# Performance work log

Hardware: AMD Instinct MI355X
Metric: run time of the kernel (lower is better)

## Reference

```python
import jax, jax.numpy as jnp
import numpy as np

B, N, FDIM = 2, 512, 1024
HEADS, DH = 4, 256          # out_per_head = 1024 // 4
AH = 256                    # attn_hidden
HID, OUT, NCLS = 512, 128, 10
RATIO, TEMP = 0.8, 0.5


def setup_inputs() -> dict:
    key = jax.random.key(0)
    ks = jax.random.split(key, 16)
    g = lambda i, shape, s: (jax.random.normal(ks[i], shape, dtype=jnp.float32) * s)
    return {
        "x": g(0, (B, N, FDIM), 1.0),
        # GATLayer
        "Wg": g(1, (FDIM, FDIM), 0.02),          # linear weight [out,in], no bias
        "attn": g(2, (HEADS, 2 * DH), 0.05),
        # CausalAttNetV1 edge_mlp: Linear(2F,AH) -> ReLU -> Linear(AH,1)
        "W1": g(3, (AH, 2 * FDIM), 0.02),
        "b1": jnp.zeros((AH,), jnp.float32),
        "w2": g(4, (AH,), 0.05),
        "b2": jnp.zeros((), jnp.float32),
        # GCN
        "gc1_w": g(5, (HID, FDIM), 0.03), "gc1_b": jnp.zeros((HID,), jnp.float32),
        "bn1_g": jnp.ones((HID,), jnp.float32), "bn1_b": jnp.zeros((HID,), jnp.float32),
        "gc2_w": g(6, (OUT, HID), 0.04), "gc2_b": jnp.zeros((OUT,), jnp.float32),
        "bn2_g": jnp.ones((OUT,), jnp.float32), "bn2_b": jnp.zeros((OUT,), jnp.float32),
        # classifier
        "cls_w": g(7, (NCLS, OUT), 0.1), "cls_b": jnp.zeros((NCLS,), jnp.float32),
    }


def _batchnorm(h, gamma, beta):
    # BatchNorm1d in training mode over the flattened (B*N, F) dim, biased var.
    m = h.mean(axis=(0, 1))
    v = jnp.mean((h - m) ** 2, axis=(0, 1))
    return (h - m) * jax.lax.rsqrt(v + 1e-5) * gamma + beta


def _forward(x, Wg, attn, W1, b1, w2, b2,
             gc1_w, gc1_b, bn1_g, bn1_b, gc2_w, gc2_b, bn2_g, bn2_b,
             cls_w, cls_b):
    # ---- GATLayer (adj=None) ----
    hp = jnp.einsum('bnf,of->bno', x, Wg)                     # [B,N,1024]
    hp = hp.reshape(B, N, HEADS, DH).transpose(0, 2, 1, 3)     # [B,H,N,DH]
    a_i, a_j = attn[:, :DH], attn[:, DH:]
    s_i = jnp.einsum('bhnd,hd->bhn', hp, a_i)                  # source score
    s_j = jnp.einsum('bhnd,hd->bhn', hp, a_j)                  # target score
    e = s_i[:, :, :, None] + s_j[:, :, None, :]                # [B,H,N,N]
    e = jnp.where(e >= 0, e, 0.2 * e)                          # LeakyReLU(0.2)
    alpha = jax.nn.softmax(e, axis=-1)
    hn = jnp.einsum('bhij,bhjd->bhid', alpha, hp)
    node_feats = hn.transpose(0, 2, 1, 3).reshape(B, N, HEADS * DH)  # [B,N,1024]

    # ---- CausalAttNetV1 (split cat-linear into row/col halves) ----
    W1i, W1j = W1[:, :FDIM], W1[:, FDIM:]
    pi = jnp.einsum('bnf,af->bna', node_feats, W1i)            # [B,N,AH]
    pj = jnp.einsum('bnf,af->bna', node_feats, W1j)
    hid = jax.nn.relu(pi[:, :, None, :] + pj[:, None, :, :] + b1)  # [B,N,N,AH]
    edge_scores = jnp.einsum('bija,a->bij', hid, w2) + b2      # [B,N,N]
    flat = edge_scores.reshape(B, N * N)
    soft_mask = jax.nn.softmax(flat / TEMP, axis=1)
    k = int(RATIO * N * N)
    thr = jnp.sort(soft_mask, axis=1)[:, -k]                   # k-th largest value
    cm = jnp.where(soft_mask >= thr[:, None], soft_mask, 0.0)
    cm = cm / (cm.sum(axis=1, keepdims=True) + 1e-12)
    causal_adj = cm.reshape(B, N, N)

    # ---- GCN (return_embeddings=True) ----
    h = jnp.einsum('bij,bjf->bif', causal_adj, node_feats)
    h = jnp.einsum('bif,of->bio', h, gc1_w) + gc1_b
    h = jax.nn.relu(_batchnorm(h, bn1_g, bn1_b))
    h = jnp.einsum('bij,bjf->bif', causal_adj, h)
    h = jnp.einsum('bif,of->bio', h, gc2_w) + gc2_b
    h = jax.nn.relu(_batchnorm(h, bn2_g, bn2_b))

    # ---- classify (mode='pred') ----
    feat_causal = h.mean(axis=1)                               # [B,128]
    return jnp.einsum('bf,cf->bc', feat_causal, cls_w) + cls_b # [B,NCLS]


def reference(x, Wg, attn, W1, b1, w2, b2,
              gc1_w, gc1_b, bn1_g, bn1_b, gc2_w, gc2_b, bn2_g, bn2_b,
              cls_w, cls_b):
    return _forward(x, Wg, attn, W1, b1, w2, b2,
                    gc1_w, gc1_b, bn1_g, bn1_b, gc2_w, gc2_b, bn2_g, bn2_b,
                    cls_w, cls_b)
```

## Files before the change

kernel.cpp:

```cpp
#include <hip/hip_runtime.h>
#include <hip/hip_bf16.h>


__global__ __launch_bounds__(256) void gemm64_nt(
    const float* __restrict__ A, const float* __restrict__ Bm, float* __restrict__ C,
    int K, int lda, int ldb, int ldc, const float* __restrict__ bias,
    const float* __restrict__ Bm2, float* __restrict__ C2, const float* __restrict__ bias2,
    int ksplit)
{
    if (ksplit){
        int z = blockIdx.z; A += (size_t)z*K; Bm += (size_t)z*K; if (z) bias = nullptr;
    } else if (blockIdx.z){
        Bm = Bm2; C = C2; bias = bias2;
    }
    __shared__ float As[64][64], Bs[64][64];
    int t = threadIdx.x;
    int m0 = blockIdx.y*64, n0 = blockIdx.x*64;
    int w = t>>6, lane = t&63;
    int mi = lane>>3, ni = lane&7;
    int kc = w*16;
    const float* Ar = A + (size_t)(m0+lane)*lda + kc;
    const float* Br = Bm + (size_t)(n0+lane)*ldb + kc;
    float4 pa[4], pb[4];
    #pragma unroll
    for (int j=0;j<4;++j){ pa[j]=*(const float4*)(Ar+j*4); pb[j]=*(const float4*)(Br+j*4); }
    float acc[8][8] = {};
    for (int k0=0; k0<K; k0+=64){
        #pragma unroll
        for (int j=0;j<4;++j){
            As[kc+j*4+0][lane]=pa[j].x; As[kc+j*4+1][lane]=pa[j].y;
            As[kc+j*4+2][lane]=pa[j].z; As[kc+j*4+3][lane]=pa[j].w;
            Bs[kc+j*4+0][lane]=pb[j].x; Bs[kc+j*4+1][lane]=pb[j].y;
            Bs[kc+j*4+2][lane]=pb[j].z; Bs[kc+j*4+3][lane]=pb[j].w;
        }
        if (k0+64 < K){
            #pragma unroll
            for (int j=0;j<4;++j){
                pa[j]=*(const float4*)(Ar+k0+64+j*4);
                pb[j]=*(const float4*)(Br+k0+64+j*4);
            }
        }
        #pragma unroll
        for (int kk=0; kk<16; ++kk){
            float4 a0=*(const float4*)&As[kc+kk][mi*8], a1=*(const float4*)&As[kc+kk][mi*8+4];
            float4 b0=*(const float4*)&Bs[kc+kk][ni*8], b1=*(const float4*)&Bs[kc+kk][ni*8+4];
            float am[8]={a0.x,a0.y,a0.z,a0.w,a1.x,a1.y,a1.z,a1.w};
            float bn[8]={b0.x,b0.y,b0.z,b0.w,b1.x,b1.y,b1.z,b1.w};
            #pragma unroll
            for (int i=0;i<8;++i)
                #pragma unroll
                for (int j2=0;j2<8;++j2) acc[i][j2] += am[i]*bn[j2];
        }
    }
    __syncthreads();
    float* s0 = &As[0][0]; float* s1 = &Bs[0][0];
    if (w>=2){
        float* d = (w==2)? s0 : s1;
        #pragma unroll
        for (int i=0;i<8;++i){
            *(float4*)&d[(mi*8+i)*64+ni*8]   = make_float4(acc[i][0],acc[i][1],acc[i][2],acc[i][3]);
            *(float4*)&d[(mi*8+i)*64+ni*8+4] = make_float4(acc[i][4],acc[i][5],acc[i][6],acc[i][7]);
        }
    }
    __syncthreads();
    if (w<2){
        const float* sv = (w==0)? s0 : s1;
        #pragma unroll
        for (int i=0;i<8;++i){
            float4 v0=*(const float4*)&sv[(mi*8+i)*64+ni*8];
            float4 v1=*(const float4*)&sv[(mi*8+i)*64+ni*8+4];
            acc[i][0]+=v0.x; acc[i][1]+=v0.y; acc[i][2]+=v0.z; acc[i][3]+=v0.w;
            acc[i][4]+=v1.x; acc[i][5]+=v1.y; acc[i][6]+=v1.z; acc[i][7]+=v1.w;
        }
    }
    __syncthreads();
    if (w==1){
        #pragma unroll
        for (int i=0;i<8;++i){
            *(float4*)&s0[(mi*8+i)*64+ni*8]   = make_float4(acc[i][0],acc[i][1],acc[i][2],acc[i][3]);
            *(float4*)&s0[(mi*8+i)*64+ni*8+4] = make_float4(acc[i][4],acc[i][5],acc[i][6],acc[i][7]);
        }
    }
    __syncthreads();
    if (w==0){
        #pragma unroll
        for (int i=0;i<8;++i){
            float4 v0=*(const float4*)&s0[(mi*8+i)*64+ni*8];
            float4 v1=*(const float4*)&s0[(mi*8+i)*64+ni*8+4];
            acc[i][0]+=v0.x; acc[i][1]+=v0.y; acc[i][2]+=v0.z; acc[i][3]+=v0.w;
            acc[i][4]+=v1.x; acc[i][5]+=v1.y; acc[i][6]+=v1.z; acc[i][7]+=v1.w;
        }
        float bb[8];
        #pragma unroll
        for (int j2=0;j2<8;++j2) bb[j2] = bias ? bias[n0+ni*8+j2] : 0.f;
        if (!ksplit){
            #pragma unroll
            for (int i=0;i<8;++i){
                *(float4*)&C[(size_t)(m0+mi*8+i)*ldc + n0+ni*8]   =
                    make_float4(acc[i][0]+bb[0],acc[i][1]+bb[1],acc[i][2]+bb[2],acc[i][3]+bb[3]);
                *(float4*)&C[(size_t)(m0+mi*8+i)*ldc + n0+ni*8+4] =
                    make_float4(acc[i][4]+bb[4],acc[i][5]+bb[5],acc[i][6]+bb[6],acc[i][7]+bb[7]);
            }
        } else {
            #pragma unroll
            for (int i=0;i<8;++i)
                #pragma unroll
                for (int j2=0;j2<8;++j2)
                    atomicAdd(&C[(size_t)(m0+mi*8+i)*ldc + n0+ni*8+j2], acc[i][j2]+bb[j2]);
        }
    }
}

__global__ __launch_bounds__(256) void gemm64_nn(
    const float* __restrict__ A, const float* __restrict__ Bm, float* __restrict__ C,
    int K, int lda, int ldb, int ldc, long sA, long sB, long sC,
    const float* __restrict__ bsc, const float* __restrict__ bsh)
{
    A += (long)blockIdx.z*sA; Bm += (long)blockIdx.z*sB; C += (long)blockIdx.z*sC;
    __shared__ float As[64][64], Bs[64][64];
    int t=threadIdx.x, w=t>>6, lane=t&63;
    int m0=blockIdx.y*64, n0=blockIdx.x*64;
    int mi=lane>>3, ni=lane&7;
    int kc=w*16;
    const float* Ar = A + (size_t)(m0+lane)*lda + kc;
    int kr = lane>>4, nc = (lane&15)*4;
    const float* Br = Bm + (size_t)(kc+kr)*ldb + n0 + nc;
    float4 sc4 = make_float4(1,1,1,1), sh4 = make_float4(0,0,0,0);
    if (bsc){ sc4 = *(const float4*)&bsc[n0+nc]; sh4 = *(const float4*)&bsh[n0+nc]; }
    float4 pa[4], pb[4];
    #pragma unroll
    for (int j=0;j<4;++j){
        pa[j]=*(const float4*)(Ar+j*4);
        pb[j]=*(const float4*)(Br + (size_t)(j*4)*ldb);
    }
    float acc[8][8] = {};
    for (int k0=0; k0<K; k0+=64){
        #pragma unroll
        for (int j=0;j<4;++j){
            As[kc+j*4+0][lane]=pa[j].x; As[kc+j*4+1][lane]=pa[j].y;
            As[kc+j*4+2][lane]=pa[j].z; As[kc+j*4+3][lane]=pa[j].w;
            float4 bv = pb[j];
            if (bsc){
                bv.x=fmaxf(bv.x*sc4.x+sh4.x,0.f); bv.y=fmaxf(bv.y*sc4.y+sh4.y,0.f);
                bv.z=fmaxf(bv.z*sc4.z+sh4.z,0.f); bv.w=fmaxf(bv.w*sc4.w+sh4.w,0.f);
            }
            *(float4*)&Bs[kc+kr+j*4][nc] = bv;
        }
        if (k0+64 < K){
            #pragma unroll
            for (int j=0;j<4;++j){
                pa[j]=*(const float4*)(Ar+k0+64+j*4);
                pb[j]=*(const float4*)(Br + (size_t)(k0+64+j*4)*ldb);
            }
        }
        #pragma unroll
        for (int kk=0; kk<16; ++kk){
            float4 a0=*(const float4*)&As[kc+kk][mi*8], a1=*(const float4*)&As[kc+kk][mi*8+4];
            float4 b0=*(const float4*)&Bs[kc+kk][ni*8], b1=*(const float4*)&Bs[kc+kk][ni*8+4];
            float am[8]={a0.x,a0.y,a0.z,a0.w,a1.x,a1.y,a1.z,a1.w};
            float bn[8]={b0.x,b0.y,b0.z,b0.w,b1.x,b1.y,b1.z,b1.w};
            #pragma unroll
            for (int i=0;i<8;++i)
                #pragma unroll
                for (int j2=0;j2<8;++j2) acc[i][j2] += am[i]*bn[j2];
        }
    }
    __syncthreads();
    float* s0 = &As[0][0]; float* s1 = &Bs[0][0];
    if (w>=2){
        float* d = (w==2)? s0 : s1;
        #pragma unroll
        for (int i=0;i<8;++i){
            *(float4*)&d[(mi*8+i)*64+ni*8]   = make_float4(acc[i][0],acc[i][1],acc[i][2],acc[i][3]);
            *(float4*)&d[(mi*8+i)*64+ni*8+4] = make_float4(acc[i][4],acc[i][5],acc[i][6],acc[i][7]);
        }
    }
    __syncthreads();
    if (w<2){
        const float* sv = (w==0)? s0 : s1;
        #pragma unroll
        for (int i=0;i<8;++i){
            float4 v0=*(const float4*)&sv[(mi*8+i)*64+ni*8];
            float4 v1=*(const float4*)&sv[(mi*8+i)*64+ni*8+4];
            acc[i][0]+=v0.x; acc[i][1]+=v0.y; acc[i][2]+=v0.z; acc[i][3]+=v0.w;
            acc[i][4]+=v1.x; acc[i][5]+=v1.y; acc[i][6]+=v1.z; acc[i][7]+=v1.w;
        }
    }
    __syncthreads();
    if (w==1){
        #pragma unroll
        for (int i=0;i<8;++i){
            *(float4*)&s0[(mi*8+i)*64+ni*8]   = make_float4(acc[i][0],acc[i][1],acc[i][2],acc[i][3]);
            *(float4*)&s0[(mi*8+i)*64+ni*8+4] = make_float4(acc[i][4],acc[i][5],acc[i][6],acc[i][7]);
        }
    }
    __syncthreads();
    if (w==0){
        #pragma unroll
        for (int i=0;i<8;++i){
            float4 v0=*(const float4*)&s0[(mi*8+i)*64+ni*8];
            float4 v1=*(const float4*)&s0[(mi*8+i)*64+ni*8+4];
            acc[i][0]+=v0.x; acc[i][1]+=v0.y; acc[i][2]+=v0.z; acc[i][3]+=v0.w;
            acc[i][4]+=v1.x; acc[i][5]+=v1.y; acc[i][6]+=v1.z; acc[i][7]+=v1.w;
        }
        #pragma unroll
        for (int i=0;i<8;++i){
            *(float4*)&C[(size_t)(m0+mi*8+i)*ldc + n0+ni*8]   =
                make_float4(acc[i][0],acc[i][1],acc[i][2],acc[i][3]);
            *(float4*)&C[(size_t)(m0+mi*8+i)*ldc + n0+ni*8+4] =
                make_float4(acc[i][4],acc[i][5],acc[i][6],acc[i][7]);
        }
    }
}

__global__ void transp_v15(const float* __restrict__ PJ, float* __restrict__ pjT){
    __shared__ float T[64][68];
    int b = blockIdx.z;
    int a0 = blockIdx.x*64, n0 = blockIdx.y*64;
    int t = threadIdx.x;
    int c = t&15, r = t>>4;
    for (int rr=r; rr<64; rr+=16){
        float4 v = *(const float4*)&PJ[(size_t)(b*512+n0+rr)*256 + a0 + c*4];
        T[rr][c*4]=v.x; T[rr][c*4+1]=v.y; T[rr][c*4+2]=v.z; T[rr][c*4+3]=v.w;
    }
    __syncthreads();
    for (int rr=r; rr<64; rr+=16){
        float4 o = make_float4(T[c*4][rr], T[c*4+1][rr], T[c*4+2][rr], T[c*4+3][rr]);
        *(float4*)&pjT[(size_t)b*131072 + (size_t)(a0+rr)*512 + n0 + c*4] = o;
    }
}

__global__ void bnp1(const float* __restrict__ src, float* __restrict__ PS,
                     float* __restrict__ PS2, int F){
    int f0 = blockIdx.x*64, r0 = blockIdx.y*64;
    int fi = threadIdx.x & 63, rg = threadIdx.x >> 6;
    float s=0.f, s2=0.f;
    #pragma unroll
    for (int i=0;i<16;++i){
        float v = src[(size_t)(r0+rg+i*4)*F + f0+fi];
        s += v; s2 += v*v;
    }
    __shared__ float ls[4][64], ls2[4][64];
    ls[rg][fi]=s; ls2[rg][fi]=s2; __syncthreads();
    if (rg==0){
        PS [blockIdx.y*F + f0+fi] = ls[0][fi]+ls[1][fi]+ls[2][fi]+ls[3][fi];
        PS2[blockIdx.y*F + f0+fi] = ls2[0][fi]+ls2[1][fi]+ls2[2][fi]+ls2[3][fi];
    }
}

__global__ void bnp2(const float* __restrict__ PS, const float* __restrict__ PS2,
                     const float* __restrict__ g, const float* __restrict__ be,
                     float* __restrict__ scale, float* __restrict__ shift, int F){
    int f = blockIdx.x*64 + threadIdx.x;
    float S=0.f, S2=0.f;
    #pragma unroll
    for (int c=0;c<16;++c){ S += PS[c*F+f]; S2 += PS2[c*F+f]; }
    float m  = S*(1.f/1024.f);
    float var = S2*(1.f/1024.f) - m*m;
    float sc = g[f] * rsqrtf(var + 1e-5f);
    scale[f]=sc; shift[f]=be[f] - m*sc;
}

__global__ void feat_p(const float* __restrict__ h4, const float* __restrict__ sc,
                       const float* __restrict__ sh, float* __restrict__ featp){
    int b = blockIdx.x, chunk = blockIdx.y;
    int t = threadIdx.x;
    float s = sc[t], o = sh[t], acc = 0.f;
    int n0 = chunk*64;
    #pragma unroll
    for (int i=0;i<64;++i){
        float v = h4[(size_t)(b*512+n0+i)*128 + t]*s + o;
        acc += fmaxf(v, 0.f);
    }
    featp[(b*8+chunk)*128 + t] = acc;
}

__global__ void feat_f(const float* __restrict__ featp, float* __restrict__ feat){
    int b = blockIdx.x, t = threadIdx.x;
    float a = 0.f;
    #pragma unroll
    for (int c=0;c<8;++c) a += featp[(b*8+c)*128 + t];
    feat[b*128+t] = a*(1.f/512.f);
}

__global__ void gemm_nn32(const float* __restrict__ A, const float* __restrict__ Bm,
                          float* __restrict__ C, int K, int lda, int ldb, int ldc,
                          long sA, long sB, long sC,
                          const float* __restrict__ bsc, const float* __restrict__ bsh){
    A  += (long)blockIdx.z * sA;
    Bm += (long)blockIdx.z * sB;
    C  += (long)blockIdx.z * sC;
    __shared__ float As[16][32], Bs[16][64];
    int n0 = blockIdx.x*64, m0 = blockIdx.y*32;
    int t = threadIdx.x, tx = t & 15, ty = t >> 4;
    int sr = t >> 3, sk = (t & 7)*2;
    int bk = t >> 4, bn4 = (t & 15)*4;
    float acc[2][4] = {};
    for (int k0=0; k0<K; k0+=16){
        #pragma unroll
        for (int i=0;i<2;++i) As[sk+i][sr] = A[(size_t)(m0+sr)*lda + k0+sk+i];
        float4 bv = *(const float4*)&Bm[(size_t)(k0+bk)*ldb + n0+bn4];
        if (bsc){
            bv.x = fmaxf(bv.x*bsc[n0+bn4+0]+bsh[n0+bn4+0], 0.f);
            bv.y = fmaxf(bv.y*bsc[n0+bn4+1]+bsh[n0+bn4+1], 0.f);
            bv.z = fmaxf(bv.z*bsc[n0+bn4+2]+bsh[n0+bn4+2], 0.f);
            bv.w = fmaxf(bv.w*bsc[n0+bn4+3]+bsh[n0+bn4+3], 0.f);
        }
        *(float4*)&Bs[bk][bn4] = bv;
        __syncthreads();
        #pragma unroll
        for (int k=0;k<16;++k){
            float a0 = As[k][ty*2], a1 = As[k][ty*2+1];
            float4 b = *(const float4*)&Bs[k][tx*4];
            acc[0][0]+=a0*b.x; acc[0][1]+=a0*b.y; acc[0][2]+=a0*b.z; acc[0][3]+=a0*b.w;
            acc[1][0]+=a1*b.x; acc[1][1]+=a1*b.y; acc[1][2]+=a1*b.z; acc[1][3]+=a1*b.w;
        }
        __syncthreads();
    }
    #pragma unroll
    for (int i=0;i<2;++i){
        float4 v = make_float4(acc[i][0],acc[i][1],acc[i][2],acc[i][3]);
        *(float4*)&C[(size_t)(m0+ty*2+i)*ldc + n0+tx*4] = v;
    }
}

__global__ void gemm_nt32(const float* __restrict__ A, const float* __restrict__ Bm,
                          float* __restrict__ C, int K, int lda, int ldb, int ldc,
                          const float* __restrict__ bias){
    __shared__ float As[16][32], Bs[16][64];
    int n0 = blockIdx.x*64, m0 = blockIdx.y*32;
    int t = threadIdx.x, tx = t & 15, ty = t >> 4;
    int sr = t >> 3, sk = (t & 7)*2;
    int bn = t >> 2, bkk = (t & 3)*4;
    float acc[2][4] = {};
    for (int k0=0; k0<K; k0+=16){
        #pragma unroll
        for (int i=0;i<2;++i) As[sk+i][sr] = A[(size_t)(m0+sr)*lda + k0+sk+i];
        float4 wv = *(const float4*)&Bm[(size_t)(n0+bn)*ldb + k0+bkk];
        Bs[bkk+0][bn]=wv.x; Bs[bkk+1][bn]=wv.y; Bs[bkk+2][bn]=wv.z; Bs[bkk+3][bn]=wv.w;
        __syncthreads();
        #pragma unroll
        for (int k=0;k<16;++k){
            float a0 = As[k][ty*2], a1 = As[k][ty*2+1];
            float4 b = *(const float4*)&Bs[k][tx*4];
            acc[0][0]+=a0*b.x; acc[0][1]+=a0*b.y; acc[0][2]+=a0*b.z; acc[0][3]+=a0*b.w;
            acc[1][0]+=a1*b.x; acc[1][1]+=a1*b.y; acc[1][2]+=a1*b.z; acc[1][3]+=a1*b.w;
        }
        __syncthreads();
    }
    float4 bb = bias ? *(const float4*)&bias[n0+tx*4] : make_float4(0,0,0,0);
    #pragma unroll
    for (int i=0;i<2;++i){
        float4 v = make_float4(acc[i][0]+bb.x,acc[i][1]+bb.y,acc[i][2]+bb.z,acc[i][3]+bb.w);
        *(float4*)&C[(size_t)(m0+ty*2+i)*ldc + n0+tx*4] = v;
    }
}

__global__ void gemm_x_v12(const float* __restrict__ X, const float* __restrict__ Wg,
                           float* __restrict__ dst){
    __shared__ float xs[4][1024];
    int m0 = blockIdx.x*4;
    int t = threadIdx.x;
    for (int i=t;i<4096;i+=256){ int r=i>>10, c=i&1023; xs[r][c]=X[(size_t)(m0+r)*1024+c]; }
    __syncthreads();
    const float* w0 = Wg + (size_t)(t*4)*1024;
    float acc[4][4] = {};
    for (int k0=0;k0<1024;k0+=16){
        float4 xv[4][4];
        #pragma unroll
        for (int r=0;r<4;++r)
            #pragma unroll
            for (int c=0;c<4;++c) xv[r][c] = *(const float4*)&xs[r][k0+4*c];
        #pragma unroll
        for (int j=0;j<4;++j){
            const float* wr = w0 + (size_t)j*1024 + k0;
            #pragma unroll
            for (int c=0;c<4;++c){
                float4 w = *(const float4*)(wr + 4*c);
                #pragma unroll
                for (int r=0;r<4;++r)
                    acc[r][j] += xv[r][c].x*w.x + xv[r][c].y*w.y
                               + xv[r][c].z*w.z + xv[r][c].w*w.w;
            }
        }
    }
    int n0 = t*4;
    #pragma unroll
    for (int r=0;r<4;++r){
        float4 v = make_float4(acc[r][0],acc[r][1],acc[r][2],acc[r][3]);
        *(float4*)&dst[(size_t)(m0+r)*1024 + n0] = v;
    }
}

__global__ void attn_v12(const float* __restrict__ hp, const float* __restrict__ attn,
                         float* __restrict__ nf){
    int blk = blockIdx.x;
    int bh = blk >> 6, i0 = (blk & 63)*8;
    int b = bh >> 2, h = bh & 3;
    int t = threadIdx.x;
    __shared__ float ais[256], ajs[256], sjs[512], sis[8], inv[8];
    __shared__ float alpha[8][512];
    __shared__ float red[256];
    ais[t] = attn[h*512 + t];
    ajs[t] = attn[h*512 + 256 + t];
    __syncthreads();
    const float* hpb = hp + (size_t)b*524288 + h*256;
    for (int j=t; j<512; j+=256){
        const float* row = hpb + (size_t)j*1024;
        float s=0.f;
        for (int d=0; d<256; ++d) s += row[d]*ajs[d];
        sjs[j]=s;
    }
    if (t<8){
        const float* row = hpb + (size_t)(i0+t)*1024;
        float s=0.f;
        for (int d=0; d<256; ++d) s += row[d]*ais[d];
        sis[t]=s;
    }
    __syncthreads();
    for (int ii=0; ii<8; ++ii){
        float si = sis[ii];
        float e0 = si + sjs[t], e1 = si + sjs[t+256];
        e0 = (e0>=0.f)? e0 : 0.2f*e0;
        e1 = (e1>=0.f)? e1 : 0.2f*e1;
        float p0 = expf(e0), p1 = expf(e1);
        alpha[ii][t]=p0; alpha[ii][t+256]=p1;
        red[t]=p0+p1; __syncthreads();
        for (int s=128; s>0; s>>=1){ if (t<s) red[t]+=red[t+s]; __syncthreads(); }
        if (t==0) inv[ii] = 1.0f/red[0];
        __syncthreads();
    }
    float acc[8] = {};
    for (int j=0; j<512; ++j){
        float r = hpb[(size_t)j*1024 + t];
        #pragma unroll
        for (int ii=0; ii<8; ++ii) acc[ii] += alpha[ii][j]*r;
    }
    #pragma unroll
    for (int ii=0; ii<8; ++ii)
        nf[(size_t)(b*512+i0+ii)*1024 + h*256 + t] = acc[ii]*inv[ii];
}

__global__ void sij_v14(const float* __restrict__ hp, const float* __restrict__ attn,
                        float* __restrict__ SI, float* __restrict__ SJ){
    int t = threadIdx.x;
    int lane = t & 63, w = t >> 6;
    int h  = lane >> 4;
    int e0 = (lane & 15) * 16;
    const float* ai = attn + h*512 + e0;
    const float* aj = ai + 256;
    float4 wi[4], wj[4];
    #pragma unroll
    for (int q=0;q<4;++q){ wi[q] = *(const float4*)(ai + 4*q); wj[q] = *(const float4*)(aj + 4*q); }
    int row0 = blockIdx.x*16 + w*4;
    for (int r=0;r<4;++r){
        int row = row0 + r;
        const float* hr = hp + (size_t)row*1024 + h*256 + e0;
        float si=0.f, sj=0.f;
        #pragma unroll
        for (int q=0;q<4;++q){
            float4 v = *(const float4*)(hr + 4*q);
            si += v.x*wi[q].x + v.y*wi[q].y + v.z*wi[q].z + v.w*wi[q].w;
            sj += v.x*wj[q].x + v.y*wj[q].y + v.z*wj[q].z + v.w*wj[q].w;
        }
        #pragma unroll
        for (int s=1;s<16;s<<=1){
            si += __shfl_xor(si, s, 64);
            sj += __shfl_xor(sj, s, 64);
        }
        if ((lane & 15)==0){
            int b = row >> 9, n = row & 511;
            SI[(size_t)(b*4+h)*512 + n] = si;
            SJ[(size_t)(b*4+h)*512 + n] = sj;
        }
    }
}

__global__ __launch_bounds__(512) void attn_pv_v16(const float* __restrict__ hp,
                                                   const float* __restrict__ SI,
                                                   const float* __restrict__ SJ,
                                                   float* __restrict__ nf){
    int blk = blockIdx.x;
    int bh = blk >> 5, i0 = (blk & 31)*16;
    int b = bh >> 2, h = bh & 3;
    int t = threadIdx.x;
    int w = t >> 6, lane = t & 63;
    __shared__ float alpha[16][512];
    __shared__ float wsum[8][16];
    __shared__ float inv[16];
    const float* sjp = SJ + (size_t)bh*512;
    float sj = sjp[t];
    const float* sip = SI + (size_t)bh*512 + i0;
    float part[16];
    #pragma unroll
    for (int ii=0; ii<16; ++ii){
        float e = sip[ii] + sj;
        e = (e>=0.f)? e : 0.2f*e;
        float p = expf(e);
        alpha[ii][t] = p;
        part[ii] = p;
    }
    #pragma unroll
    for (int s=1;s<64;s<<=1){
        #pragma unroll
        for (int ii=0;ii<16;++ii) part[ii] += __shfl_xor(part[ii], s, 64);
    }
    if (lane==0){
        #pragma unroll
        for (int ii=0;ii<16;++ii) wsum[w][ii] = part[ii];
    }
    __syncthreads();
    if (t<16){
        float s=0.f;
        #pragma unroll
        for (int ww=0;ww<8;++ww) s += wsum[ww][t];
        inv[t] = 1.0f/s;
    }
    __syncthreads();
    int d0 = lane*4;
    int iA = w*2;
    const float* hpb = hp + (size_t)b*524288 + h*256 + d0;
    float4 acc0 = make_float4(0,0,0,0), acc1 = make_float4(0,0,0,0);
    for (int j=0; j<512; j+=4){
        float4 r0 = *(const float4*)&hpb[(size_t)(j+0)*1024];
        float4 r1 = *(const float4*)&hpb[(size_t)(j+1)*1024];
        float4 r2 = *(const float4*)&hpb[(size_t)(j+2)*1024];
        float4 r3 = *(const float4*)&hpb[(size_t)(j+3)*1024];
        float4 a0 = *(const float4*)&alpha[iA][j];
        float4 a1 = *(const float4*)&alpha[iA+1][j];
        acc0.x += a0.x*r0.x + a0.y*r1.x + a0.z*r2.x + a0.w*r3.x;
        acc0.y += a0.x*r0.y + a0.y*r1.y + a0.z*r2.y + a0.w*r3.y;
        acc0.z += a0.x*r0.z + a0.y*r1.z + a0.z*r2.z + a0.w*r3.z;
        acc0.w += a0.x*r0.w + a0.y*r1.w + a0.z*r2.w + a0.w*r3.w;
        acc1.x += a1.x*r0.x + a1.y*r1.x + a1.z*r2.x + a1.w*r3.x;
        acc1.y += a1.x*r0.y + a1.y*r1.y + a1.z*r2.y + a1.w*r3.y;
        acc1.z += a1.x*r0.z + a1.y*r1.z + a1.z*r2.z + a1.w*r3.z;
        acc1.w += a1.x*r0.w + a1.y*r1.w + a1.z*r2.w + a1.w*r3.w;
    }
    float v0 = inv[iA], v1 = inv[iA+1];
    *(float4*)&nf[(size_t)(b*512+i0+iA  )*1024 + h*256 + d0] =
        make_float4(acc0.x*v0, acc0.y*v0, acc0.z*v0, acc0.w*v0);
    *(float4*)&nf[(size_t)(b*512+i0+iA+1)*1024 + h*256 + d0] =
        make_float4(acc1.x*v1, acc1.y*v1, acc1.z*v1, acc1.w*v1);
}

__global__ void pipj_v13(const float* __restrict__ nf, const float* __restrict__ W1,
                         const float* __restrict__ b1, float* __restrict__ pi,
                         float* __restrict__ pjT){
    int half = blockIdx.z >> 5;
    int m0 = (blockIdx.z & 31)*32;
    int a0 = blockIdx.x*64;
    __shared__ float As[16][32], Bs[16][64];
    int t = threadIdx.x, tx = t & 15, ty = t >> 4;
    int sr = t >> 3, sk = (t & 7)*2;
    int bn = t >> 2, bkk = (t & 3)*4;
    const float* Wbase = W1 + (half ? 1024 : 0);
    float acc[2][4] = {};
    for (int k0=0; k0<1024; k0+=16){
        #pragma unroll
        for (int i=0;i<2;++i) As[sk+i][sr] = nf[(size_t)(m0+sr)*1024 + k0+sk+i];
        float4 wv = *(const float4*)&Wbase[(size_t)(a0+bn)*2048 + k0+bkk];
        Bs[bkk+0][bn]=wv.x; Bs[bkk+1][bn]=wv.y; Bs[bkk+2][bn]=wv.z; Bs[bkk+3][bn]=wv.w;
        __syncthreads();
        #pragma unroll
        for (int k=0;k<16;++k){
            float a0v = As[k][ty*2], a1v = As[k][ty*2+1];
            float4 b = *(const float4*)&Bs[k][tx*4];
            acc[0][0]+=a0v*b.x; acc[0][1]+=a0v*b.y; acc[0][2]+=a0v*b.z; acc[0][3]+=a0v*b.w;
            acc[1][0]+=a1v*b.x; acc[1][1]+=a1v*b.y; acc[1][2]+=a1v*b.z; acc[1][3]+=a1v*b.w;
        }
        __syncthreads();
    }
    if (!half){
        float4 bb = *(const float4*)&b1[a0+tx*4];
        #pragma unroll
        for (int i=0;i<2;++i){
            float4 v = make_float4(acc[i][0]+bb.x,acc[i][1]+bb.y,acc[i][2]+bb.z,acc[i][3]+bb.w);
            *(float4*)&pi[(size_t)(m0+ty*2+i)*256 + a0+tx*4] = v;
        }
    } else {
        #pragma unroll
        for (int i=0;i<2;++i){
            int m = m0+ty*2+i;
            size_t base = (size_t)(m>>9)*131072 + (m&511);
            #pragma unroll
            for (int j=0;j<4;++j)
                pjT[base + (size_t)(a0+tx*4+j)*512] = acc[i][j];
        }
    }
}

__global__ void edge_v10(const float* __restrict__ pi, const float* __restrict__ pjT,
                         const float* __restrict__ w2, const float* __restrict__ b2,
                         float* __restrict__ es){
    int blk = blockIdx.x;
    int b = blk >> 8, i0 = (blk & 255)*2;
    int t = threadIdx.x;
    __shared__ float pis[2][256], w2s[256];
    w2s[t] = w2[t];
    pis[0][t] = pi[(size_t)(b*512+i0)*256 + t];
    pis[1][t] = pi[(size_t)(b*512+i0+1)*256 + t];
    __syncthreads();
    float a00=0,a01=0,a10=0,a11=0;
    const float* pj = pjT + (size_t)b*131072;
    for (int a=0; a<256; ++a){
        float pv0 = pj[(size_t)a*512 + t];
        float pv1 = pj[(size_t)a*512 + t + 256];
        float w  = w2s[a];
        a00 += fmaxf(pis[0][a]+pv0, 0.f)*w;
        a01 += fmaxf(pis[0][a]+pv1, 0.f)*w;
        a10 += fmaxf(pis[1][a]+pv0, 0.f)*w;
        a11 += fmaxf(pis[1][a]+pv1, 0.f)*w;
    }
    float b2f = b2[0];
    es[(size_t)(b*512+i0+0)*512 + t]       = a00 + b2f;
    es[(size_t)(b*512+i0+0)*512 + t + 256] = a01 + b2f;
    es[(size_t)(b*512+i0+1)*512 + t]       = a10 + b2f;
    es[(size_t)(b*512+i0+1)*512 + t + 256] = a11 + b2f;
}

__global__ void k_exp_v13(float* __restrict__ u, float* __restrict__ S){
    int b = blockIdx.x >> 8;
    size_t base = (size_t)b*262144 + (size_t)(blockIdx.x & 255)*1024;
    int t = threadIdx.x;
    float acc = 0.f;
    for (int i=t;i<1024;i+=256){ float v = expf(u[base+i]*2.0f); u[base+i]=v; acc+=v; }
    __shared__ float red[256];
    red[t]=acc; __syncthreads();
    for (int s=128;s>0;s>>=1){ if(t<s) red[t]+=red[t+s]; __syncthreads(); }
    if (t==0) atomicAdd(&S[b], red[0]);
}

__global__ void k_hist_v11(const float* __restrict__ u, unsigned* __restrict__ hist,
                           const unsigned* __restrict__ pfx, int cmpShift, int shift,
                           unsigned mask, int nbins){
    __shared__ unsigned h[2048];
    for (int i=threadIdx.x;i<nbins;i+=256) h[i]=0;
    __syncthreads();
    int b = blockIdx.x>>6;
    size_t base = (size_t)b*262144 + (size_t)(blockIdx.x&63)*4096;
    unsigned p = pfx ? pfx[b] : 0u;
    for (int i=threadIdx.x;i<4096;i+=256){
        unsigned bits = __float_as_uint(u[base+i]);
        if (!pfx || (bits>>cmpShift)==p) atomicAdd(&h[(bits>>shift)&mask],1u);
    }
    __syncthreads();
    for (int i=threadIdx.x;i<nbins;i+=256) if (h[i]) atomicAdd(&hist[b*nbins+i], h[i]);
}

__global__ void k_scan_v11(const unsigned* __restrict__ hist, int nbins,
                           unsigned* __restrict__ pfx, unsigned* __restrict__ rank,
                           int passBits, int first, float* __restrict__ thrOut){
    __shared__ unsigned part[2][256];
    int batch = threadIdx.x>>8, lane = threadIdx.x&255;
    int chunk = nbins/256;
    const unsigned* hb = hist + batch*nbins;
    unsigned s=0;
    for (int i=0;i<chunk;++i) s += hb[lane*chunk+i];
    part[batch][lane]=s;
    __syncthreads();
    if (lane==0){
        unsigned r = first ? 52429u : rank[batch];
        unsigned cum=0; int c=0;
        for (;c<256;++c){ unsigned pc=part[batch][c]; if (cum+pc>r) break; cum+=pc; }
        if (c==256) c=255;
        int bin=c*chunk;
        for (int i=0;i<chunk;++i){ unsigned cnt=hb[c*chunk+i]; if (cum+cnt>r){ bin=c*chunk+i; break;} cum+=cnt; }
        rank[batch]=r-cum;
        unsigned np = ((first?0u:pfx[batch])<<passBits) | (unsigned)bin;
        pfx[batch]=np;
        if (thrOut) thrOut[batch]=__uint_as_float(np);
    }
}

__global__ void k_csum_v11(const float* __restrict__ u, const float* __restrict__ THR,
                           float* __restrict__ CS, unsigned* __restrict__ KC){
    int b = blockIdx.x>>6;
    size_t base = (size_t)b*262144 + (size_t)(blockIdx.x&63)*4096;
    float th = THR[b];
    float cs=0.f; unsigned kc=0;
    for (int i=threadIdx.x;i<4096;i+=256){ float v=u[base+i]; if (v>=th){ cs+=v; kc++; } }
    __shared__ float rf[256]; __shared__ unsigned ru[256];
    rf[threadIdx.x]=cs; ru[threadIdx.x]=kc; __syncthreads();
    for (int s=128;s>0;s>>=1){ if(threadIdx.x<s){ rf[threadIdx.x]+=rf[threadIdx.x+s]; ru[threadIdx.x]+=ru[threadIdx.x+s]; } __syncthreads(); }
    if (threadIdx.x==0){ atomicAdd(&CS[b], rf[0]); atomicAdd(&KC[b], ru[0]); }
}

__global__ void k_fin_v11(const float* __restrict__ S, const float* __restrict__ CS,
                          const unsigned* __restrict__ KC, float* __restrict__ THR,
                          float* __restrict__ DINV){
    int t = threadIdx.x;
    if (t < 2){
        float ks = CS[t]; float th = THR[t];
        if (KC[t] < 209715u){ th = 0.f; ks = S[t]; }
        THR[t]=th;
        DINV[t]=1.0f/(ks + 1e-12f*S[t]);
    }
}

__global__ void adj_v10(float* __restrict__ u, const float* __restrict__ thrU,
                        const float* __restrict__ dinv){
    int idx = blockIdx.x*256 + threadIdx.x;
    int b = idx >> 18;
    float v = u[idx];
    u[idx] = (v >= thrU[b]) ? v*dinv[b] : 0.0f;
}

__global__ void bnstats_v10(const float* __restrict__ src, const float* __restrict__ g,
                            const float* __restrict__ be, float* __restrict__ scale,
                            float* __restrict__ shift, int F){
    int f0 = blockIdx.x*64;
    int fi = threadIdx.x & 63, rg = threadIdx.x >> 6;
    float s=0.f, s2=0.f;
    for (int r=rg; r<1024; r+=4){ float v = src[(size_t)r*F + f0+fi]; s+=v; s2+=v*v; }
    __shared__ float ls[4][64], ls2[4][64];
    ls[rg][fi]=s; ls2[rg][fi]=s2; __syncthreads();
    if (rg==0){
        float Sv = ls[0][fi]+ls[1][fi]+ls[2][fi]+ls[3][fi];
        float S2 = ls2[0][fi]+ls2[1][fi]+ls2[2][fi]+ls2[3][fi];
        float m  = Sv*(1.f/1024.f);
        float var = S2*(1.f/1024.f) - m*m;
        float sc = g[f0+fi] * rsqrtf(var + 1e-5f);
        scale[f0+fi]=sc;
        shift[f0+fi]=be[f0+fi] - m*sc;
    }
}

__global__ void feat_v10(const float* __restrict__ h4, const float* __restrict__ sc,
                         const float* __restrict__ sh, float* __restrict__ feat){
    int b = blockIdx.x, t = threadIdx.x;
    float s = sc[t], o = sh[t], acc = 0.f;
    for (int n=0; n<512; ++n){
        float v = h4[(size_t)(b*512+n)*128 + t]*s + o;
        acc += fmaxf(v, 0.f);
    }
    feat[b*128+t] = acc*(1.f/512.f);
}

__global__ void cls_v10(const float* __restrict__ feat, const float* __restrict__ cls_w,
                        const float* __restrict__ cls_b, float* __restrict__ out){
    int t = threadIdx.x;
    if (t < 20){
        int b = t/10, c = t%10;
        float acc = cls_b[c];
        for (int o=0; o<128; ++o)
            acc += feat[b*128+o]*cls_w[c*128+o];
        out[t] = acc;
    }
}

extern "C" void kernel_launch(void* const* d_in, const int* in_sizes, int n_in,
                              void* d_out, int out_size, void* d_ws, size_t ws_size,
                              hipStream_t stream){
    (void)in_sizes; (void)n_in; (void)out_size;
    const float* x     = (const float*)d_in[0];
    const float* Wg    = (const float*)d_in[1];
    const float* attn  = (const float*)d_in[2];
    const float* W1    = (const float*)d_in[3];
    const float* b1    = (const float*)d_in[4];
    const float* w2    = (const float*)d_in[5];
    const float* b2    = (const float*)d_in[6];
    const float* gc1_w = (const float*)d_in[7];
    const float* gc1_b = (const float*)d_in[8];
    const float* bn1_g = (const float*)d_in[9];
    const float* bn1_b = (const float*)d_in[10];
    const float* gc2_w = (const float*)d_in[11];
    const float* gc2_b = (const float*)d_in[12];
    const float* bn2_g = (const float*)d_in[13];
    const float* bn2_b = (const float*)d_in[14];
    const float* cls_w = (const float*)d_in[15];
    const float* cls_b = (const float*)d_in[16];
    float* out = (float*)d_out;

    float *HP, *NF, *U, *PI, *PJT, *H1, *H2, *H3, *H4;
    float *STAT, *BN1S, *BN1H, *BN2S, *BN2H, *FEAT;
    float *SIbuf = nullptr, *SJbuf = nullptr, *PJ = nullptr;
    float *PSb = nullptr, *PS2b = nullptr, *FEATP = nullptr;
    int wsPath = (ws_size >= (size_t)22*1024*1024);

    if (wsPath){
        float* W = (float*)d_ws;
        HP  = W + 0;        NF  = W + 1048576;  H1 = W + 2097152;
        PI  = W + 3145728;  PJT = W + 3407872;  U  = W + 3670016;
        H2  = W + 4194304;  H3  = W + 4718592;  H4 = W + 5242880;
        BN1S= W + 5374208;  BN1H= W + 5374720;
        BN2S= W + 5375232;  BN2H= W + 5375360;  FEAT = W + 5375488;
        STAT= W + 5400000;
        SIbuf = W + 5500000; SJbuf = W + 5504096;
        PJ  = H2;
        PSb = W + 5420000; PS2b = W + 5430000; FEATP = W + 5440000;
    } else {
        HP  = (float*)x;
        NF  = (float*)Wg;
        PI  = (float*)x;
        PJT = (float*)x + 262144;
        U   = (float*)W1;
        H1  = (float*)x;
        H2  = (float*)Wg;
        H3  = (float*)gc1_w;
        H4  = (float*)x;
        STAT= (float*)x;
        float* A = (float*)attn;
        BN1S = A+8;    BN1H = A+520;
        BN2S = A+1032; BN2H = A+1160;  FEAT = A+1288;
    }
    float*    S    = STAT+2;
    float*    CS   = STAT+4;
    unsigned* KC   = (unsigned*)(STAT+6);
    unsigned* PFX  = (unsigned*)(STAT+8);
    unsigned* RANK = (unsigned*)(STAT+10);
    float*    THR  = STAT+12;
    float*    DINV = STAT+14;
    unsigned* H0   = (unsigned*)(STAT+16);
    unsigned* Hh1  = (unsigned*)(STAT+16+4096);
    unsigned* Hh2  = (unsigned*)(STAT+16+8192);

    if (wsPath){
        gemm64_nt<<<dim3(16,16,1),256,0,stream>>>(x, Wg, HP, 1024, 1024, 1024, 1024,
                                                  nullptr, nullptr, nullptr, nullptr, 0);
        sij_v14    <<<64,256,0,stream>>>(HP, attn, SIbuf, SJbuf);
        attn_pv_v16<<<256,512,0,stream>>>(HP, SIbuf, SJbuf, NF);
        gemm64_nt<<<dim3(4,16,2),256,0,stream>>>(NF, W1, PI, 1024, 1024, 2048, 256,
                                                 b1, W1+1024, PJ, nullptr, 0);
        transp_v15<<<dim3(4,8,2),256,0,stream>>>(PJ, PJT);
    } else {
        gemm_x_v12<<<256,256,0,stream>>>(x, Wg, HP);
        attn_v12  <<<512,256,0,stream>>>(HP, attn, NF);
        pipj_v13  <<<dim3(4,1,64),256,0,stream>>>(NF, W1, b1, PI, PJT);
    }
    edge_v10  <<<512,256,0,stream>>>(PI, PJT, w2, b2, U);
    hipMemsetAsync(STAT, 0, 10256*sizeof(float), stream);
    if (wsPath) hipMemsetAsync(H4, 0, 131072*sizeof(float), stream);
    k_exp_v13 <<<512,256,0,stream>>>(U, S);
    k_hist_v11<<<128,256,0,stream>>>(U, H0, nullptr, 0, 21, 0x7FFu, 2048);
    k_scan_v11<<<1,512,0,stream>>>(H0, 2048, PFX, RANK, 11, 1, nullptr);
    k_hist_v11<<<128,256,0,stream>>>(U, Hh1, PFX, 21, 10, 0x7FFu, 2048);
    k_scan_v11<<<1,512,0,stream>>>(Hh1, 2048, PFX, RANK, 11, 0, nullptr);
    k_hist_v11<<<128,256,0,stream>>>(U, Hh2, PFX, 10, 0, 0x3FFu, 1024);
    k_scan_v11<<<1,512,0,stream>>>(Hh2, 1024, PFX, RANK, 10, 0, THR);
    k_csum_v11<<<128,256,0,stream>>>(U, THR, CS, KC);
    k_fin_v11 <<<1,64,0,stream>>>(S, CS, KC, THR, DINV);
    adj_v10   <<<2048,256,0,stream>>>(U, THR, DINV);

    if (wsPath){
        gemm64_nn<<<dim3(16,8,2),256,0,stream>>>(U, NF, H1, 512, 512, 1024, 1024,
                                                 262144, 524288, 524288, nullptr, nullptr);
        gemm64_nt<<<dim3(8,16,1),256,0,stream>>>(H1, gc1_w, H2, 1024, 1024, 1024, 512,
                                                 gc1_b, nullptr, nullptr, nullptr, 0);
        bnp1<<<dim3(8,16),256,0,stream>>>(H2, PSb, PS2b, 512);
        bnp2<<<8,64,0,stream>>>(PSb, PS2b, bn1_g, bn1_b, BN1S, BN1H, 512);
        gemm64_nn<<<dim3(8,8,2),256,0,stream>>>(U, H2, H3, 512, 512, 512, 512,
                                                262144, 262144, 262144, BN1S, BN1H);
        gemm64_nt<<<dim3(2,16,4),256,0,stream>>>(H3, gc2_w, H4, 128, 512, 512, 128,
                                                 gc2_b, nullptr, nullptr, nullptr, 1);
        bnp1<<<dim3(2,16),256,0,stream>>>(H4, PSb, PS2b, 128);
        bnp2<<<2,64,0,stream>>>(PSb, PS2b, bn2_g, bn2_b, BN2S, BN2H, 128);
        feat_p<<<dim3(2,8),128,0,stream>>>(H4, BN2S, BN2H, FEATP);
        feat_f<<<2,128,0,stream>>>(FEATP, FEAT);
    } else {
        gemm_nn32 <<<dim3(16,16,2),256,0,stream>>>(U, NF, H1, 512, 512, 1024, 1024,
                                                   262144, 524288, 524288, nullptr, nullptr);
        gemm_nt32 <<<dim3(8,32),256,0,stream>>>(H1, gc1_w, H2, 1024, 1024, 1024, 512, gc1_b);
        bnstats_v10<<<8,256,0,stream>>>(H2, bn1_g, bn1_b, BN1S, BN1H, 512);
        gemm_nn32 <<<dim3(8,16,2),256,0,stream>>>(U, H2, H3, 512, 512, 512, 512,
                                                  262144, 262144, 262144, BN1S, BN1H);
        gemm_nt32 <<<dim3(2,32),256,0,stream>>>(H3, gc2_w, H4, 512, 512, 512, 128, gc2_b);
        bnstats_v10<<<2,256,0,stream>>>(H4, bn2_g, bn2_b, BN2S, BN2H, 128);
        feat_v10  <<<2,128,0,stream>>>(H4, BN2S, BN2H, FEAT);
    }
    cls_v10   <<<1,64,0,stream>>>(FEAT, cls_w, cls_b, out);
}
```

Measured before the change: 411.9 us.

## Split GAT attention into softmax materialization plus tiled batched GEMM

The fused attention kernel that computed softmax weights into shared memory and then streamed HP rows with per-thread dot products is replaced by two steps. A kernel first writes normalized alpha matrices [B*H,512,512] to a workspace buffer aliased on PI. The existing 64x64 tiled gemm64_nn kernel then computes alpha·HP per (batch, head) through a new head-offset mode. This aims for better register and shared-memory reuse of HP in the PV product, at the cost of an extra 8 MB write and read of alpha plus one more launch.

```diff
diff --git a/kernel.cpp b/kernel.cpp
--- a/kernel.cpp
+++ b/kernel.cpp
@@ -114,9 +114,16 @@
 __global__ __launch_bounds__(256) void gemm64_nn(
     const float* __restrict__ A, const float* __restrict__ Bm, float* __restrict__ C,
     int K, int lda, int ldb, int ldc, long sA, long sB, long sC,
-    const float* __restrict__ bsc, const float* __restrict__ bsh)
+    const float* __restrict__ bsc, const float* __restrict__ bsh, int bhmode)
 {
-    A += (long)blockIdx.z*sA; Bm += (long)blockIdx.z*sB; C += (long)blockIdx.z*sC;
+    if (bhmode){
+        int z = blockIdx.z;
+        A  += (size_t)z*sA;
+        Bm += (size_t)(z>>2)*sB + (size_t)(z&3)*256;
+        C  += (size_t)(z>>2)*sC + (size_t)(z&3)*256;
+    } else {
+        A += (long)blockIdx.z*sA; Bm += (long)blockIdx.z*sB; C += (long)blockIdx.z*sC;
+    }
     __shared__ float As[64][64], Bs[64][64];
     int t=threadIdx.x, w=t>>6, lane=t&63;
     int m0=blockIdx.y*64, n0=blockIdx.x*64;
@@ -476,29 +483,24 @@
     }
 }
 
-__global__ __launch_bounds__(512) void attn_pv_v16(const float* __restrict__ hp,
-                                                   const float* __restrict__ SI,
-                                                   const float* __restrict__ SJ,
-                                                   float* __restrict__ nf){
+__global__ __launch_bounds__(512) void asm_v17(const float* __restrict__ SI,
+                                               const float* __restrict__ SJ,
+                                               float* __restrict__ ALP){
     int blk = blockIdx.x;
     int bh = blk >> 5, i0 = (blk & 31)*16;
-    int b = bh >> 2, h = bh & 3;
     int t = threadIdx.x;
     int w = t >> 6, lane = t & 63;
-    __shared__ float alpha[16][512];
     __shared__ float wsum[8][16];
     __shared__ float inv[16];
-    const float* sjp = SJ + (size_t)bh*512;
-    float sj = sjp[t];
+    float sj = SJ[(size_t)bh*512 + t];
     const float* sip = SI + (size_t)bh*512 + i0;
-    float part[16];
+    float p[16], part[16];
     #pragma unroll
     for (int ii=0; ii<16; ++ii){
         float e = sip[ii] + sj;
         e = (e>=0.f)? e : 0.2f*e;
-        float p = expf(e);
-        alpha[ii][t] = p;
-        part[ii] = p;
+        p[ii] = expf(e);
+        part[ii] = p[ii];
     }
     #pragma unroll
     for (int s=1;s<64;s<<=1){
@@ -517,31 +519,10 @@
         inv[t] = 1.0f/s;
     }
     __syncthreads();
-    int d0 = lane*4;
-    int iA = w*2;
-    const float* hpb = hp + (size_t)b*524288 + h*256 + d0;
-    float4 acc0 = make_float4(0,0,0,0), acc1 = make_float4(0,0,0,0);
-    for (int j=0; j<512; j+=4){
-        float4 r0 = *(const float4*)&hpb[(size_t)(j+0)*1024];
-        float4 r1 = *(const float4*)&hpb[(size_t)(j+1)*1024];
-        float4 r2 = *(const float4*)&hpb[(size_t)(j+2)*1024];
-        float4 r3 = *(const float4*)&hpb[(size_t)(j+3)*1024];
-        float4 a0 = *(const float4*)&alpha[iA][j];
-        float4 a1 = *(const float4*)&alpha[iA+1][j];
-        acc0.x += a0.x*r0.x + a0.y*r1.x + a0.z*r2.x + a0.w*r3.x;
-        acc0.y += a0.x*r0.y + a0.y*r1.y + a0.z*r2.y + a0.w*r3.y;
-        acc0.z += a0.x*r0.z + a0.y*r1.z + a0.z*r2.z + a0.w*r3.z;
-        acc0.w += a0.x*r0.w + a0.y*r1.w + a0.z*r2.w + a0.w*r3.w;
-        acc1.x += a1.x*r0.x + a1.y*r1.x + a1.z*r2.x + a1.w*r3.x;
-        acc1.y += a1.x*r0.y + a1.y*r1.y + a1.z*r2.y + a1.w*r3.y;
-        acc1.z += a1.x*r0.z + a1.y*r1.z + a1.z*r2.z + a1.w*r3.z;
-        acc1.w += a1.x*r0.w + a1.y*r1.w + a1.z*r2.w + a1.w*r3.w;
-    }
-    float v0 = inv[iA], v1 = inv[iA+1];
-    *(float4*)&nf[(size_t)(b*512+i0+iA  )*1024 + h*256 + d0] =
-        make_float4(acc0.x*v0, acc0.y*v0, acc0.z*v0, acc0.w*v0);
-    *(float4*)&nf[(size_t)(b*512+i0+iA+1)*1024 + h*256 + d0] =
-        make_float4(acc1.x*v1, acc1.y*v1, acc1.z*v1, acc1.w*v1);
+    float* dst = ALP + (size_t)bh*262144 + (size_t)i0*512 + t;
+    #pragma unroll
+    for (int ii=0; ii<16; ++ii)
+        dst[(size_t)ii*512] = p[ii]*inv[ii];
 }
 
 __global__ void pipj_v13(const float* __restrict__ nf, const float* __restrict__ W1,
@@ -774,7 +755,7 @@
 
     float *HP, *NF, *U, *PI, *PJT, *H1, *H2, *H3, *H4;
     float *STAT, *BN1S, *BN1H, *BN2S, *BN2H, *FEAT;
-    float *SIbuf = nullptr, *SJbuf = nullptr, *PJ = nullptr;
+    float *SIbuf = nullptr, *SJbuf = nullptr, *PJ = nullptr, *ALP = nullptr;
     float *PSb = nullptr, *PS2b = nullptr, *FEATP = nullptr;
     int wsPath = (ws_size >= (size_t)22*1024*1024);
 
@@ -788,6 +769,7 @@
         STAT= W + 5400000;
         SIbuf = W + 5500000; SJbuf = W + 5504096;
         PJ  = H2;
+        ALP = PI;
         PSb = W + 5420000; PS2b = W + 5430000; FEATP = W + 5440000;
     } else {
         HP  = (float*)x;
@@ -818,8 +800,10 @@
     if (wsPath){
         gemm64_nt<<<dim3(16,16,1),256,0,stream>>>(x, Wg, HP, 1024, 1024, 1024, 1024,
                                                   nullptr, nullptr, nullptr, nullptr, 0);
-        sij_v14    <<<64,256,0,stream>>>(HP, attn, SIbuf, SJbuf);
-        attn_pv_v16<<<256,512,0,stream>>>(HP, SIbuf, SJbuf, NF);
+        sij_v14 <<<64,256,0,stream>>>(HP, attn, SIbuf, SJbuf);
+        asm_v17 <<<256,512,0,stream>>>(SIbuf, SJbuf, ALP);
+        gemm64_nn<<<dim3(4,8,8),256,0,stream>>>(ALP, HP, NF, 512, 512, 1024, 1024,
+                                                262144, 524288, 524288, nullptr, nullptr, 1);
         gemm64_nt<<<dim3(4,16,2),256,0,stream>>>(NF, W1, PI, 1024, 1024, 2048, 256,
                                                  b1, W1+1024, PJ, nullptr, 0);
         transp_v15<<<dim3(4,8,2),256,0,stream>>>(PJ, PJT);
@@ -844,13 +828,13 @@
 
     if (wsPath){
         gemm64_nn<<<dim3(16,8,2),256,0,stream>>>(U, NF, H1, 512, 512, 1024, 1024,
-                                                 262144, 524288, 524288, nullptr, nullptr);
+                                                 262144, 524288, 524288, nullptr, nullptr, 0);
         gemm64_nt<<<dim3(8,16,1),256,0,stream>>>(H1, gc1_w, H2, 1024, 1024, 1024, 512,
                                                  gc1_b, nullptr, nullptr, nullptr, 0);
         bnp1<<<dim3(8,16),256,0,stream>>>(H2, PSb, PS2b, 512);
         bnp2<<<8,64,0,stream>>>(PSb, PS2b, bn1_g, bn1_b, BN1S, BN1H, 512);
         gemm64_nn<<<dim3(8,8,2),256,0,stream>>>(U, H2, H3, 512, 512, 512, 512,
-                                                262144, 262144, 262144, BN1S, BN1H);
+                                                262144, 262144, 262144, BN1S, BN1H, 0);
         gemm64_nt<<<dim3(2,16,4),256,0,stream>>>(H3, gc2_w, H4, 128, 512, 512, 128,
                                                  gc2_b, nullptr, nullptr, nullptr, 1);
         bnp1<<<dim3(2,16),256,0,stream>>>(H4, PSb, PS2b, 128);
```

Result: faster. 386.3 us (-6.2%).
